# Optimization experiments

Hardware: AMD Instinct MI355X
Metric: run time of the kernel (lower is better)

Reference implementation:

```python
import jax, jax.numpy as jnp
import numpy as np

B, N, M = 32, 4096, 32
IN_F, OUT_F, A = 256, 256, 8


def setup_inputs() -> dict:
    key = jax.random.key(0)
    k1, k2, k3, k4, k5 = jax.random.split(key, 5)
    fatoms = jax.random.normal(k1, (B, N, IN_F), dtype=jnp.float32)
    agraph = jax.random.randint(k2, (B, N, M), 0, N, dtype=jnp.int64)
    anchor_indices = jax.random.randint(k3, (B, A), 0, N, dtype=jnp.int64)
    # xavier-uniform-like init for W and a
    wlim = float(np.sqrt(6.0 / (IN_F + OUT_F)))
    alim = float(np.sqrt(6.0 / (2 * OUT_F + 1)))
    W = jax.random.uniform(k4, (IN_F, OUT_F), dtype=jnp.float32, minval=-wlim, maxval=wlim)
    a = jax.random.uniform(k5, (2 * OUT_F, 1), dtype=jnp.float32, minval=-alim, maxval=alim)
    return {"fatoms": fatoms, "agraph": agraph, "anchor_indices": anchor_indices, "W": W, "a": a}


def reference(fatoms, agraph, anchor_indices, W, a):
    # h: (B, N, F)
    h = jnp.matmul(fatoms, W)
    F_ = h.shape[-1]
    # gather anchor features: (B, A, F)
    anchor_feat = jnp.take_along_axis(h, anchor_indices[:, :, None], axis=1)
    # e = cat([h_self + h_anch, h_self - h_anch]) @ a, decomposed to avoid the
    # (B, N, A, 2F) intermediate: e = h @ (a1+a2) + h_anch @ (a1-a2)
    a1 = a[:F_, 0]
    a2 = a[F_:, 0]
    e = (h @ (a1 + a2))[:, :, None] + (anchor_feat @ (a1 - a2))[:, None, :]  # (B, N, A)
    # mask[b,n,k] = anchor_indices[b,k] in agraph[b,n,:]  (vectorized torch.isin)
    mask = (agraph[:, :, None, :] == anchor_indices[:, None, :, None]).any(axis=-1)  # (B, N, A)
    e = jnp.where(mask, e, jnp.float32(-1e9))
    attn = jax.nn.softmax(e, axis=-1)
    # weighted sum of anchor features: (B, N, F)
    return jnp.einsum('bna,baf->bnf', attn, anchor_feat)
```

## Files before the change

### kernel.cpp

```cpp
#include <hip/hip_runtime.h>

#define B_ 32
#define N_ 4096
#define M_ 32
#define F_ 256
#define A_ 8

typedef float f32x4 __attribute__((ext_vector_type(4)));
typedef int   i32x4 __attribute__((ext_vector_type(4)));

#define WS_AF 0
#define WS_E2 (B_ * A_ * F_)

__global__ __launch_bounds__(256) void anchor_kernel(const float* __restrict__ fatoms,
                                                     const int* __restrict__ anchor_idx,
                                                     const float* __restrict__ W,
                                                     const float* __restrict__ a,
                                                     float* __restrict__ ws) {
    int bk = blockIdx.x;
    int b  = bk / A_;
    int f  = threadIdx.x;
    __shared__ float xs[F_];
    __shared__ float red[F_];
    int idx = anchor_idx[bk];
    xs[f] = fatoms[((size_t)b * N_ + idx) * F_ + f];
    __syncthreads();
    float acc[4] = {0.f, 0.f, 0.f, 0.f};
    for (int i0 = 0; i0 < F_; i0 += 16) {
#pragma unroll
        for (int j = 0; j < 16; ++j)
            acc[j & 3] += xs[i0 + j] * W[(i0 + j) * F_ + f];
    }
    float accs = (acc[0] + acc[1]) + (acc[2] + acc[3]);
    ws[WS_AF + bk * F_ + f] = accs;
    red[f] = accs * (a[f] - a[f + F_]);
    __syncthreads();
    for (int s = 128; s > 0; s >>= 1) {
        if (f < s) red[f] += red[f + s];
        __syncthreads();
    }
    if (f == 0) ws[WS_E2 + bk] = red[0];
}

#define RPW 64

__global__ __launch_bounds__(64) void main_kernel(const int* __restrict__ agraph,
                                                  const int* __restrict__ anchor_idx,
                                                  const float* __restrict__ ws,
                                                  float* __restrict__ out) {
    int lane = threadIdx.x;
    const int chunks_per_batch = N_ / RPW;
    int b     = blockIdx.x / chunks_per_batch;
    int chunk = blockIdx.x % chunks_per_batch;
    int row0  = chunk * RPW;

    const i32x4* gp = (const i32x4*)(agraph + ((size_t)b * N_ + row0 + lane) * M_);
    i32x4 g[M_ / 4];
#pragma unroll
    for (int j = 0; j < M_ / 4; ++j) g[j] = gp[j];

    const float* af = ws + WS_AF + b * (A_ * F_);
    const float* e2 = ws + WS_E2 + b * A_;

    __shared__ float attn[RPW][A_];
    __shared__ unsigned char flags[RPW];

    int   anch[A_];
    float e2r[A_];
#pragma unroll
    for (int k = 0; k < A_; ++k) {
        anch[k] = anchor_idx[b * A_ + k];
        e2r[k]  = e2[k];
    }
    float m8 = e2r[0];
#pragma unroll
    for (int k = 1; k < A_; ++k) m8 = fmaxf(m8, e2r[k]);
    float E[A_];
#pragma unroll
    for (int k = 0; k < A_; ++k) E[k] = __expf(e2r[k] - m8);

    f32x4 afr[A_];
#pragma unroll
    for (int k = 0; k < A_; ++k) afr[k] = *(const f32x4*)(af + k * F_ + lane * 4);
    f32x4 afm = ((afr[0] + afr[1]) + (afr[2] + afr[3])) +
                ((afr[4] + afr[5]) + (afr[6] + afr[7]));
    afm *= 0.125f;

    {
        unsigned mk = 0;
#pragma unroll
        for (int j = 0; j < M_ / 4; ++j) {
#pragma unroll
            for (int k = 0; k < A_; ++k) {
                int hit = (g[j].x == anch[k]) | (g[j].y == anch[k]) |
                          (g[j].z == anch[k]) | (g[j].w == anch[k]);
                mk |= hit ? (1u << k) : 0u;
            }
        }
        flags[lane] = (unsigned char)(mk ? 1u : 0u);
        if (mk) {
            float p[A_], s = 0.f;
#pragma unroll
            for (int k = 0; k < A_; ++k) { p[k] = (mk & (1u << k)) ? E[k] : 0.f; s += p[k]; }
            float rinv = __builtin_amdgcn_rcpf(s);
            f32x4 pa = {p[0] * rinv, p[1] * rinv, p[2] * rinv, p[3] * rinv};
            f32x4 pb = {p[4] * rinv, p[5] * rinv, p[6] * rinv, p[7] * rinv};
            *(f32x4*)&attn[lane][0] = pa;
            *(f32x4*)&attn[lane][4] = pb;
        }
    }
    __syncthreads();

    size_t base = ((size_t)b * N_ + row0) * F_ + lane * 4;
    for (int r0 = 0; r0 < RPW; r0 += 4) {
        unsigned f4 = *(const unsigned*)&flags[r0];
        f32x4 o[4];
        if (f4 == 0) {
#pragma unroll
            for (int u = 0; u < 4; ++u) o[u] = afm;
        } else {
#pragma unroll
            for (int u = 0; u < 4; ++u) {
                if ((f4 >> (8 * u)) & 0xffu) {
                    f32x4 pa = *(const f32x4*)&attn[r0 + u][0];
                    f32x4 pb = *(const f32x4*)&attn[r0 + u][4];
                    f32x4 t = pa.x * afr[0];
                    t += pa.y * afr[1];
                    t += pa.z * afr[2];
                    t += pa.w * afr[3];
                    t += pb.x * afr[4];
                    t += pb.y * afr[5];
                    t += pb.z * afr[6];
                    t += pb.w * afr[7];
                    o[u] = t;
                } else {
                    o[u] = afm;
                }
            }
        }
#pragma unroll
        for (int u = 0; u < 4; ++u)
            *(f32x4*)(out + base + (size_t)(r0 + u) * F_) = o[u];
    }
}

extern "C" void kernel_launch(void* const* d_in, const int* in_sizes, int n_in,
                              void* d_out, int out_size, void* d_ws, size_t ws_size,
                              hipStream_t stream) {
    const float* fatoms     = (const float*)d_in[0];
    const int*   agraph     = (const int*)d_in[1];
    const int*   anchor_idx = (const int*)d_in[2];
    const float* W          = (const float*)d_in[3];
    const float* a          = (const float*)d_in[4];
    float*       out        = (float*)d_out;
    float*       ws         = (float*)d_ws;

    hipLaunchKernelGGL(anchor_kernel, dim3(B_ * A_), dim3(256), 0, stream,
                       fatoms, anchor_idx, W, a, ws);
    hipLaunchKernelGGL(main_kernel, dim3(B_ * (N_ / RPW)), dim3(64), 0, stream,
                       agraph, anchor_idx, ws, out);
}
```

Measured before the change: 37.03 us.

## Move mask computation into prep kernel and stream outputs from per-row flag bytes

The agraph mask scan moves from the output kernel into the first kernel. It runs as extra blocks alongside the anchor projection blocks and writes a per-row anchor bitmask byte to workspace. The output kernel then only reads 64 flag bytes per block and recomputes the softmax weights in registers from the bitmask, removing the shared-memory attention buffer and the barrier. This overlaps the agraph read with the tiny anchor GEMV and makes the second kernel a pure store stream. In exchange it adds a round-trip of the flags through global memory and redundant per-lane softmax arithmetic.

Result: faster. 35.86 us (-3.2%).

```diff
diff --git a/kernel.cpp b/kernel.cpp
--- a/kernel.cpp
+++ b/kernel.cpp
@@ -11,82 +11,56 @@
 
 #define WS_AF 0
 #define WS_E2 (B_ * A_ * F_)
+#define WS_FLAGS_F (WS_E2 + B_ * A_)
 
-__global__ __launch_bounds__(256) void anchor_kernel(const float* __restrict__ fatoms,
-                                                     const int* __restrict__ anchor_idx,
-                                                     const float* __restrict__ W,
-                                                     const float* __restrict__ a,
-                                                     float* __restrict__ ws) {
-    int bk = blockIdx.x;
-    int b  = bk / A_;
-    int f  = threadIdx.x;
-    __shared__ float xs[F_];
-    __shared__ float red[F_];
-    int idx = anchor_idx[bk];
-    xs[f] = fatoms[((size_t)b * N_ + idx) * F_ + f];
-    __syncthreads();
-    float acc[4] = {0.f, 0.f, 0.f, 0.f};
-    for (int i0 = 0; i0 < F_; i0 += 16) {
+#define MASK_BLOCKS (B_ * N_ / 256)
+
+__global__ __launch_bounds__(256) void prep_kernel(const float* __restrict__ fatoms,
+                                                   const int* __restrict__ agraph,
+                                                   const int* __restrict__ anchor_idx,
+                                                   const float* __restrict__ W,
+                                                   const float* __restrict__ a,
+                                                   float* __restrict__ ws,
+                                                   unsigned char* __restrict__ flags) {
+    int tid = threadIdx.x;
+
+    if (blockIdx.x < (unsigned)(B_ * A_)) {
+        int bk = blockIdx.x;
+        int b  = bk / A_;
+        __shared__ float xs[F_];
+        __shared__ float red[F_];
+        int idx = anchor_idx[bk];
+        xs[tid] = fatoms[((size_t)b * N_ + idx) * F_ + tid];
+        __syncthreads();
+        float acc[4] = {0.f, 0.f, 0.f, 0.f};
+        for (int i0 = 0; i0 < F_; i0 += 16) {
 #pragma unroll
-        for (int j = 0; j < 16; ++j)
-            acc[j & 3] += xs[i0 + j] * W[(i0 + j) * F_ + f];
-    }
-    float accs = (acc[0] + acc[1]) + (acc[2] + acc[3]);
-    ws[WS_AF + bk * F_ + f] = accs;
-    red[f] = accs * (a[f] - a[f + F_]);
-    __syncthreads();
-    for (int s = 128; s > 0; s >>= 1) {
-        if (f < s) red[f] += red[f + s];
+            for (int j = 0; j < 16; ++j)
+                acc[j & 3] += xs[i0 + j] * W[(i0 + j) * F_ + tid];
+        }
+        float accs = (acc[0] + acc[1]) + (acc[2] + acc[3]);
+        ws[WS_AF + bk * F_ + tid] = accs;
+        red[tid] = accs * (a[tid] - a[tid + F_]);
         __syncthreads();
-    }
-    if (f == 0) ws[WS_E2 + bk] = red[0];
-}
+        for (int s = 128; s > 0; s >>= 1) {
+            if (tid < s) red[tid] += red[tid + s];
+            __syncthreads();
+        }
+        if (tid == 0) ws[WS_E2 + bk] = red[0];
+    } else {
+        int mb   = blockIdx.x - B_ * A_;
+        int b    = mb >> 4;
+        int gidx = mb * 256 + tid;
 
-#define RPW 64
+        int anch[A_];
+#pragma unroll
+        for (int k = 0; k < A_; ++k) anch[k] = anchor_idx[b * A_ + k];
 
-__global__ __launch_bounds__(64) void main_kernel(const int* __restrict__ agraph,
-                                                  const int* __restrict__ anchor_idx,
-                                                  const float* __restrict__ ws,
-                                                  float* __restrict__ out) {
-    int lane = threadIdx.x;
-    const int chunks_per_batch = N_ / RPW;
-    int b     = blockIdx.x / chunks_per_batch;
-    int chunk = blockIdx.x % chunks_per_batch;
-    int row0  = chunk * RPW;
+        const i32x4* gp = (const i32x4*)(agraph + (size_t)gidx * M_);
+        i32x4 g[M_ / 4];
+#pragma unroll
+        for (int j = 0; j < M_ / 4; ++j) g[j] = gp[j];
 
-    const i32x4* gp = (const i32x4*)(agraph + ((size_t)b * N_ + row0 + lane) * M_);
-    i32x4 g[M_ / 4];
-#pragma unroll
-    for (int j = 0; j < M_ / 4; ++j) g[j] = gp[j];
-
-    const float* af = ws + WS_AF + b * (A_ * F_);
-    const float* e2 = ws + WS_E2 + b * A_;
-
-    __shared__ float attn[RPW][A_];
-    __shared__ unsigned char flags[RPW];
-
-    int   anch[A_];
-    float e2r[A_];
-#pragma unroll
-    for (int k = 0; k < A_; ++k) {
-        anch[k] = anchor_idx[b * A_ + k];
-        e2r[k]  = e2[k];
-    }
-    float m8 = e2r[0];
-#pragma unroll
-    for (int k = 1; k < A_; ++k) m8 = fmaxf(m8, e2r[k]);
-    float E[A_];
-#pragma unroll
-    for (int k = 0; k < A_; ++k) E[k] = __expf(e2r[k] - m8);
-
-    f32x4 afr[A_];
-#pragma unroll
-    for (int k = 0; k < A_; ++k) afr[k] = *(const f32x4*)(af + k * F_ + lane * 4);
-    f32x4 afm = ((afr[0] + afr[1]) + (afr[2] + afr[3])) +
-                ((afr[4] + afr[5]) + (afr[6] + afr[7]));
-    afm *= 0.125f;
-
-    {
         unsigned mk = 0;
 #pragma unroll
         for (int j = 0; j < M_ / 4; ++j) {
@@ -97,23 +71,41 @@
                 mk |= hit ? (1u << k) : 0u;
             }
         }
-        flags[lane] = (unsigned char)(mk ? 1u : 0u);
-        if (mk) {
-            float p[A_], s = 0.f;
+        flags[gidx] = (unsigned char)mk;
+    }
+}
+
+__global__ __launch_bounds__(64) void stream_kernel(const float* __restrict__ ws,
+                                                    const unsigned char* __restrict__ flags,
+                                                    float* __restrict__ out) {
+    int lane = threadIdx.x;
+    int b    = blockIdx.x >> 6;
+    int row0 = (int)(blockIdx.x & 63) * 64;
+
+    const float* af = ws + WS_AF + b * (A_ * F_);
+    f32x4 afr[A_];
 #pragma unroll
-            for (int k = 0; k < A_; ++k) { p[k] = (mk & (1u << k)) ? E[k] : 0.f; s += p[k]; }
-            float rinv = __builtin_amdgcn_rcpf(s);
-            f32x4 pa = {p[0] * rinv, p[1] * rinv, p[2] * rinv, p[3] * rinv};
-            f32x4 pb = {p[4] * rinv, p[5] * rinv, p[6] * rinv, p[7] * rinv};
-            *(f32x4*)&attn[lane][0] = pa;
-            *(f32x4*)&attn[lane][4] = pb;
-        }
-    }
-    __syncthreads();
+    for (int k = 0; k < A_; ++k) afr[k] = *(const f32x4*)(af + k * F_ + lane * 4);
 
+    float e2r[A_];
+#pragma unroll
+    for (int k = 0; k < A_; ++k) e2r[k] = ws[WS_E2 + b * A_ + k];
+    float m8 = e2r[0];
+#pragma unroll
+    for (int k = 1; k < A_; ++k) m8 = fmaxf(m8, e2r[k]);
+    float E[A_];
+#pragma unroll
+    for (int k = 0; k < A_; ++k) E[k] = __expf(e2r[k] - m8);
+
+    f32x4 afm = ((afr[0] + afr[1]) + (afr[2] + afr[3])) +
+                ((afr[4] + afr[5]) + (afr[6] + afr[7]));
+    afm *= 0.125f;
+
+    const unsigned* fb = (const unsigned*)(flags + (size_t)b * N_ + row0);
     size_t base = ((size_t)b * N_ + row0) * F_ + lane * 4;
-    for (int r0 = 0; r0 < RPW; r0 += 4) {
-        unsigned f4 = *(const unsigned*)&flags[r0];
+
+    for (int r0 = 0; r0 < 64; r0 += 4) {
+        unsigned f4 = fb[r0 >> 2];
         f32x4 o[4];
         if (f4 == 0) {
 #pragma unroll
@@ -121,17 +113,23 @@
         } else {
 #pragma unroll
             for (int u = 0; u < 4; ++u) {
-                if ((f4 >> (8 * u)) & 0xffu) {
-                    f32x4 pa = *(const f32x4*)&attn[r0 + u][0];
-                    f32x4 pb = *(const f32x4*)&attn[r0 + u][4];
-                    f32x4 t = pa.x * afr[0];
-                    t += pa.y * afr[1];
-                    t += pa.z * afr[2];
-                    t += pa.w * afr[3];
-                    t += pb.x * afr[4];
-                    t += pb.y * afr[5];
-                    t += pb.z * afr[6];
-                    t += pb.w * afr[7];
+                unsigned mku = (f4 >> (8 * u)) & 0xffu;
+                if (mku) {
+                    float p[A_], s = 0.f;
+#pragma unroll
+                    for (int k = 0; k < A_; ++k) {
+                        p[k] = (mku & (1u << k)) ? E[k] : 0.f;
+                        s += p[k];
+                    }
+                    float rinv = __builtin_amdgcn_rcpf(s);
+                    f32x4 t = (p[0] * rinv) * afr[0];
+                    t += (p[1] * rinv) * afr[1];
+                    t += (p[2] * rinv) * afr[2];
+                    t += (p[3] * rinv) * afr[3];
+                    t += (p[4] * rinv) * afr[4];
+                    t += (p[5] * rinv) * afr[5];
+                    t += (p[6] * rinv) * afr[6];
+                    t += (p[7] * rinv) * afr[7];
                     o[u] = t;
                 } else {
                     o[u] = afm;
@@ -154,9 +152,10 @@
     const float* a          = (const float*)d_in[4];
     float*       out        = (float*)d_out;
     float*       ws         = (float*)d_ws;
+    unsigned char* flags    = (unsigned char*)(ws + WS_FLAGS_F);
 
-    hipLaunchKernelGGL(anchor_kernel, dim3(B_ * A_), dim3(256), 0, stream,
-                       fatoms, anchor_idx, W, a, ws);
-    hipLaunchKernelGGL(main_kernel, dim3(B_ * (N_ / RPW)), dim3(64), 0, stream,
-                       agraph, anchor_idx, ws, out);
+    hipLaunchKernelGGL(prep_kernel, dim3(B_ * A_ + MASK_BLOCKS), dim3(256), 0, stream,
+                       fatoms, agraph, anchor_idx, W, a, ws, flags);
+    hipLaunchKernelGGL(stream_kernel, dim3(B_ * (N_ / 64)), dim3(64), 0, stream,
+                       ws, flags, out);
 }
```
